# Kernel optimization log

Hardware: AMD Instinct MI355X
Metric: run time of the kernel (lower is better)

## Reference

```python
import jax, jax.numpy as jnp
import numpy as np

N = 50000
D = 128
E = 625000
EPS = 1e-15
BALL_EPS = 1e-5


def _logmap0(x, c):
    # Poincare ball log map at origin: artanh(sqrt(c)||x||) * x / (sqrt(c)||x||)
    sqrt_c = jnp.sqrt(c)
    xn = jnp.clip(jnp.linalg.norm(x, axis=-1, keepdims=True), EPS)
    arg = jnp.clip(sqrt_c * xn, -1.0 + BALL_EPS, 1.0 - BALL_EPS)
    return jnp.arctanh(arg) * x / (sqrt_c * xn)


def _expmap0(u, c):
    # Poincare ball exp map at origin: tanh(sqrt(c)||u||) * u / (sqrt(c)||u||)
    sqrt_c = jnp.sqrt(c)
    un = jnp.clip(jnp.linalg.norm(u, axis=-1, keepdims=True), EPS)
    return jnp.tanh(sqrt_c * un) * u / (sqrt_c * un)


def setup_inputs() -> dict:
    key = jax.random.key(0)
    ks = jax.random.split(key, 10)
    scale = 0.01  # keep points well inside the Poincare ball
    node_embeddings = jax.random.normal(ks[0], (N, D), jnp.float32) * scale
    hist1 = jax.random.normal(ks[1], (N, D), jnp.float32) * scale
    hist2 = jax.random.normal(ks[2], (N, D), jnp.float32) * scale
    hist3 = jax.random.normal(ks[3], (N, D), jnp.float32) * scale
    lin_w = jax.random.normal(ks[4], (D, D), jnp.float32) * (1.0 / np.sqrt(D))
    lin_b = jnp.zeros((D,), jnp.float32)
    conv_w = jax.random.normal(ks[5], (D, D, 3), jnp.float32) * (1.0 / np.sqrt(3 * D))
    conv_b = jnp.zeros((D,), jnp.float32)
    curvature = jnp.array([-1.0], jnp.float32)
    edge_src = jax.random.randint(ks[6], (E,), 0, N, jnp.int32)
    edge_dst = jax.random.randint(ks[7], (E,), 0, N, jnp.int32)
    return {
        'node_embeddings': node_embeddings,
        'hist1': hist1, 'hist2': hist2, 'hist3': hist3,
        'lin_w': lin_w, 'lin_b': lin_b,
        'conv_w': conv_w, 'conv_b': conv_b,
        'curvature': curvature,
        'edge_src': edge_src, 'edge_dst': edge_dst,
    }


def reference(node_embeddings, hist1, hist2, hist3, lin_w, lin_b,
              conv_w, conv_b, curvature, edge_src, edge_dst):
    c = jnp.abs(curvature[0])

    # --- HyperbolicDiffusionGraphConv ---
    tangent = _logmap0(node_embeddings, c)                       # [N, D]
    transformed = tangent @ lin_w.T + lin_b                      # [N, D]
    msgs = transformed[edge_src]                                 # [E, D] gather
    summed = jax.ops.segment_sum(msgs, edge_dst, num_segments=N)  # [N, D] scatter
    deg = jax.ops.segment_sum(jnp.ones((E,), jnp.float32), edge_dst, num_segments=N)
    neigh = jnp.where(deg[:, None] > 0, summed / jnp.clip(deg[:, None], 1.0), 0.0)
    current_emb = _expmap0(neigh, c)                             # [N, D]

    # --- HyperbolicDilatedCausalConv (3-step history, kernel_size=3 -> length 1) ---
    tangent_cur = _logmap0(current_emb, c)
    th = jnp.stack([_logmap0(hist1, c), _logmap0(hist2, c), _logmap0(hist3, c)], axis=2)  # [N, D, 3]
    # Conv1d(D -> D, k=3) on length-3 input reduces to a single contraction.
    conv_out = jnp.einsum('nik,oik->no', th, conv_w) + conv_b    # [N, D]
    return _expmap0(conv_out + tangent_cur, c)
```

## Files before the change

### kernel.cpp

```cpp
#include <hip/hip_runtime.h>

#define N_NODES 50000
#define DIM 128
#define N_EDGES 625000
#define EBLK2 1221
#define SLOTS 96

#define SC_BLOCKS 12500
#define PK_BLOCKS 256
#define ZR_BLOCKS 196
#define SETUP_BLOCKS (SC_BLOCKS + PK_BLOCKS + ZR_BLOCKS)

typedef float f32x4 __attribute__((ext_vector_type(4)));
typedef short s16x8 __attribute__((ext_vector_type(8)));

union U8 { unsigned short us[8]; uint4 v; };

__device__ __forceinline__ unsigned short f2bf(float f) {
    unsigned u = __builtin_bit_cast(unsigned, f);
    unsigned r = (u + 0x7fffu + ((u >> 16) & 1u)) >> 16;
    return (unsigned short)r;
}
__device__ __forceinline__ float lo_bf(unsigned u) {
    return __builtin_bit_cast(float, u << 16);
}
__device__ __forceinline__ float hi_bf(unsigned u) {
    return __builtin_bit_cast(float, u & 0xffff0000u);
}

__device__ __forceinline__ void gload_lds16(const unsigned short* g, unsigned short* l) {
    __builtin_amdgcn_global_load_lds(
        (const __attribute__((address_space(1))) void*)g,
        (__attribute__((address_space(3))) void*)l, 16, 0, 0);
}

__device__ __forceinline__ float logmap_scale(float ss, float sc) {
    float xn = fmaxf(sqrtf(ss), 1e-15f);
    float arg = fminf(sc * xn, 1.0f - 1e-5f);
    if (arg < 0.25f) {
        float z2 = arg * arg;
        return 1.0f + z2 * (0.33333333f + z2 * (0.2f + z2 * 0.14285715f));
    }
    float at = 0.5f * log1pf(2.0f * arg / (1.0f - arg));
    return at / (sc * xn);
}

__global__ __launch_bounds__(256) void k_setup(
    const float* __restrict__ node, const float* __restrict__ h1,
    const float* __restrict__ h2, const float* __restrict__ h3,
    const float* __restrict__ lin_w, const float* __restrict__ conv_w,
    const float* __restrict__ curv,
    unsigned short* __restrict__ node_t, unsigned short* __restrict__ A,
    unsigned short* __restrict__ Wt, int* __restrict__ cnt) {
    int b = blockIdx.x;
    int tid = threadIdx.x;
    if (b < SC_BLOCKS) {
        int row = b * 16 + (tid >> 4);
        int g = tid & 15;
        int a = row / N_NODES;
        int n = row - a * N_NODES;
        const float* src = (a == 0) ? node : (a == 1) ? h1 : (a == 2) ? h2 : h3;
        const float4* p = (const float4*)&src[n * DIM + g * 8];
        float4 x0 = p[0], x1 = p[1];
        float ss = x0.x * x0.x + x0.y * x0.y + x0.z * x0.z + x0.w * x0.w
                 + x1.x * x1.x + x1.y * x1.y + x1.z * x1.z + x1.w * x1.w;
        ss += __shfl_xor(ss, 1, 64);
        ss += __shfl_xor(ss, 2, 64);
        ss += __shfl_xor(ss, 4, 64);
        ss += __shfl_xor(ss, 8, 64);
        float c = fabsf(curv[0]);
        float s = logmap_scale(ss, sqrtf(c));
        U8 u;
        u.us[0] = f2bf(x0.x * s); u.us[1] = f2bf(x0.y * s);
        u.us[2] = f2bf(x0.z * s); u.us[3] = f2bf(x0.w * s);
        u.us[4] = f2bf(x1.x * s); u.us[5] = f2bf(x1.y * s);
        u.us[6] = f2bf(x1.z * s); u.us[7] = f2bf(x1.w * s);
        if (a == 0) {
            *(uint4*)&node_t[n * DIM + g * 8] = u.v;
        } else {
            *(uint4*)&A[n * 512 + a * 128 + g * 8] = u.v;
        }
    } else if (b < SC_BLOCKS + PK_BLOCKS) {
        int idx = (b - SC_BLOCKS) * 256 + tid;
        int o = idx >> 9;
        int k = idx & 511;
        float v;
        if (k < 128) {
            v = lin_w[o * 128 + k];
        } else {
            int kk = (k - 128) >> 7;
            int i = (k - 128) & 127;
            v = conv_w[o * 384 + i * 3 + kk];
        }
        Wt[idx] = f2bf(v);
    } else {
        int i = (b - SC_BLOCKS - PK_BLOCKS) * 256 + tid;
        if (i < N_NODES) cnt[i] = 0;
    }
}

__global__ void k_bucket(const int* __restrict__ esrc, const int* __restrict__ edst,
                         int* __restrict__ cnt, unsigned short* __restrict__ slots) {
    int e0 = blockIdx.x * 512 + threadIdx.x;
    int e1 = e0 + 256;
    int d0 = -1, d1 = -1, v0 = 0, v1 = 0;
    if (e0 < N_EDGES) { d0 = edst[e0]; v0 = esrc[e0]; }
    if (e1 < N_EDGES) { d1 = edst[e1]; v1 = esrc[e1]; }
    if (d0 >= 0) {
        int pos = __hip_atomic_fetch_add(&cnt[d0], 1, __ATOMIC_RELAXED,
                                         __HIP_MEMORY_SCOPE_AGENT);
        if (pos < SLOTS) slots[d0 * SLOTS + pos] = (unsigned short)v0;
    }
    if (d1 >= 0) {
        int pos = __hip_atomic_fetch_add(&cnt[d1], 1, __ATOMIC_RELAXED,
                                         __HIP_MEMORY_SCOPE_AGENT);
        if (pos < SLOTS) slots[d1 * SLOTS + pos] = (unsigned short)v1;
    }
}

__global__ __launch_bounds__(256) void k_gather(
    const unsigned short* __restrict__ slots, const int* __restrict__ cnt,
    const unsigned short* __restrict__ node_t, unsigned short* __restrict__ A) {
    int n = blockIdx.x * 8 + (threadIdx.x >> 5);
    int lane = threadIdx.x & 31;
    int ctrue = cnt[n];
    int c = ctrue < SLOTS ? ctrue : SLOTS;
    const unsigned short* row = &slots[n * SLOTS];
    float p0 = 0.f, p1 = 0.f, p2 = 0.f, p3 = 0.f;
    float q0 = 0.f, q1 = 0.f, q2 = 0.f, q3 = 0.f;
    for (int base = 0; base < c; base += 32) {
        int rem = c - base;
        int m = rem < 32 ? rem : 32;
        int my = (int)row[base + (lane < m ? lane : m - 1)];
        for (int i = 0; i < m; i += 8) {
            int i1 = i + 1 < m ? i + 1 : m - 1;
            int i2 = i + 2 < m ? i + 2 : m - 1;
            int i3 = i + 3 < m ? i + 3 : m - 1;
            int i4 = i + 4 < m ? i + 4 : m - 1;
            int i5 = i + 5 < m ? i + 5 : m - 1;
            int i6 = i + 6 < m ? i + 6 : m - 1;
            int i7 = i + 7 < m ? i + 7 : m - 1;
            int s0 = __shfl(my, i, 32),  s1 = __shfl(my, i1, 32);
            int s2 = __shfl(my, i2, 32), s3 = __shfl(my, i3, 32);
            int s4 = __shfl(my, i4, 32), s5 = __shfl(my, i5, 32);
            int s6 = __shfl(my, i6, 32), s7 = __shfl(my, i7, 32);
            uint2 u0 = *(const uint2*)&node_t[s0 * DIM + lane * 4];
            uint2 u1 = *(const uint2*)&node_t[s1 * DIM + lane * 4];
            uint2 u2 = *(const uint2*)&node_t[s2 * DIM + lane * 4];
            uint2 u3 = *(const uint2*)&node_t[s3 * DIM + lane * 4];
            uint2 u4 = *(const uint2*)&node_t[s4 * DIM + lane * 4];
            uint2 u5 = *(const uint2*)&node_t[s5 * DIM + lane * 4];
            uint2 u6 = *(const uint2*)&node_t[s6 * DIM + lane * 4];
            uint2 u7 = *(const uint2*)&node_t[s7 * DIM + lane * 4];
            p0 += lo_bf(u0.x); p1 += hi_bf(u0.x); p2 += lo_bf(u0.y); p3 += hi_bf(u0.y);
            if (i + 1 < m) { q0 += lo_bf(u1.x); q1 += hi_bf(u1.x); q2 += lo_bf(u1.y); q3 += hi_bf(u1.y); }
            if (i + 2 < m) { p0 += lo_bf(u2.x); p1 += hi_bf(u2.x); p2 += lo_bf(u2.y); p3 += hi_bf(u2.y); }
            if (i + 3 < m) { q0 += lo_bf(u3.x); q1 += hi_bf(u3.x); q2 += lo_bf(u3.y); q3 += hi_bf(u3.y); }
            if (i + 4 < m) { p0 += lo_bf(u4.x); p1 += hi_bf(u4.x); p2 += lo_bf(u4.y); p3 += hi_bf(u4.y); }
            if (i + 5 < m) { q0 += lo_bf(u5.x); q1 += hi_bf(u5.x); q2 += lo_bf(u5.y); q3 += hi_bf(u5.y); }
            if (i + 6 < m) { p0 += lo_bf(u6.x); p1 += hi_bf(u6.x); p2 += lo_bf(u6.y); p3 += hi_bf(u6.y); }
            if (i + 7 < m) { q0 += lo_bf(u7.x); q1 += hi_bf(u7.x); q2 += lo_bf(u7.y); q3 += hi_bf(u7.y); }
        }
    }
    float t0 = p0 + q0, t1 = p1 + q1, t2 = p2 + q2, t3 = p3 + q3;
    float inv = (ctrue > 0) ? 1.0f / (float)ctrue : 0.0f;
    unsigned short o0 = f2bf(t0 * inv), o1 = f2bf(t1 * inv);
    unsigned short o2 = f2bf(t2 * inv), o3 = f2bf(t3 * inv);
    uint2 ov;
    ov.x = (unsigned)o0 | ((unsigned)o1 << 16);
    ov.y = (unsigned)o2 | ((unsigned)o3 << 16);
    *(uint2*)&A[n * 512 + lane * 4] = ov;
}

#define RB 64
#define BK 64
__global__ __launch_bounds__(256) void k_gemm(
    const unsigned short* __restrict__ A, const int* __restrict__ deg,
    const unsigned short* __restrict__ Wt,
    const float* __restrict__ lin_b, const float* __restrict__ conv_b,
    const float* __restrict__ curv, float* __restrict__ out) {
    __shared__ __align__(16) unsigned short As[2][RB * BK];
    __shared__ __align__(16) unsigned short Bs[2][128 * BK];
    int tid = threadIdx.x;
    int n0 = blockIdx.x * RB;
    int w = tid >> 6;
    int lane = tid & 63;
    int ml = lane & 15;
    int q = lane >> 4;
    int lr = lane >> 3;
    int lj = lane & 7;

    f32x4 acc[8];
    #pragma unroll
    for (int i = 0; i < 8; ++i) acc[i] = (f32x4){0.f, 0.f, 0.f, 0.f};

    #pragma unroll
    for (int t = 0; t < 2; ++t) {
        int m = t * 4 + w;
        int r = m * 8 + lr;
        int jg = lj ^ (r & 7);
        gload_lds16(A + (n0 + r) * 512 + jg * 8, &As[0][m * 512]);
    }
    #pragma unroll
    for (int t = 0; t < 4; ++t) {
        int m = t * 4 + w;
        int r = m * 8 + lr;
        int jg = lj ^ (r & 7);
        gload_lds16(Wt + r * 512 + jg * 8, &Bs[0][m * 512]);
    }

    #pragma unroll
    for (int kk = 0; kk < 8; ++kk) {
        int cur = kk & 1;
        __syncthreads();
        if (kk < 7) {
            int nb = cur ^ 1;
            #pragma unroll
            for (int t = 0; t < 2; ++t) {
                int m = t * 4 + w;
                int r = m * 8 + lr;
                int jg = lj ^ (r & 7);
                gload_lds16(A + (n0 + r) * 512 + (kk + 1) * 64 + jg * 8, &As[nb][m * 512]);
            }
            #pragma unroll
            for (int t = 0; t < 4; ++t) {
                int m = t * 4 + w;
                int r = m * 8 + lr;
                int jg = lj ^ (r & 7);
                gload_lds16(Wt + r * 512 + (kk + 1) * 64 + jg * 8, &Bs[nb][m * 512]);
            }
        }
        __builtin_amdgcn_s_setprio(1);
        #pragma unroll
        for (int ks = 0; ks < 2; ++ks) {
            int ca = ((ks * 4 + q) ^ (ml & 7)) * 8;
            s16x8 a = *(const s16x8*)&As[cur][(w * 16 + ml) * BK + ca];
            #pragma unroll
            for (int ct = 0; ct < 8; ++ct) {
                s16x8 bb = *(const s16x8*)&Bs[cur][(ct * 16 + ml) * BK + ca];
                acc[ct] = __builtin_amdgcn_mfma_f32_16x16x32_bf16(a, bb, acc[ct], 0, 0, 0);
            }
        }
        __builtin_amdgcn_s_setprio(0);
    }

    float c = fabsf(curv[0]);
    float sc = sqrtf(c);
    float cb[8], lb[8];
    #pragma unroll
    for (int ct = 0; ct < 8; ++ct) {
        cb[ct] = conv_b[ct * 16 + ml];
        lb[ct] = lin_b[ct * 16 + ml];
    }
    #pragma unroll
    for (int r = 0; r < 4; ++r) {
        int n = n0 + w * 16 + q * 4 + r;
        bool valid = (n < N_NODES);
        float dgf = 0.f;
        if (valid) dgf = (deg[n] > 0) ? 1.0f : 0.0f;
        float y[8];
        float ssq = 0.f;
        #pragma unroll
        for (int ct = 0; ct < 8; ++ct) {
            float v = acc[ct][r] + cb[ct] + dgf * lb[ct];
            y[ct] = v;
            ssq += v * v;
        }
        ssq += __shfl_xor(ssq, 1, 64);
        ssq += __shfl_xor(ssq, 2, 64);
        ssq += __shfl_xor(ssq, 4, 64);
        ssq += __shfl_xor(ssq, 8, 64);
        float un = fmaxf(sqrtf(ssq), 1e-15f);
        float z = sc * un;
        float os;
        if (z < 0.25f) {
            float z2 = z * z;
            os = 1.0f + z2 * (-0.33333333f + z2 * (0.13333333f - z2 * 0.053968254f));
        } else {
            os = tanhf(z) / z;
        }
        if (valid) {
            #pragma unroll
            for (int ct = 0; ct < 8; ++ct)
                out[n * DIM + ct * 16 + ml] = y[ct] * os;
        }
    }
}

extern "C" void kernel_launch(void* const* d_in, const int* in_sizes, int n_in,
                              void* d_out, int out_size, void* d_ws, size_t ws_size,
                              hipStream_t stream) {
    (void)in_sizes; (void)n_in; (void)out_size; (void)ws_size;
    const float* node   = (const float*)d_in[0];
    const float* h1     = (const float*)d_in[1];
    const float* h2     = (const float*)d_in[2];
    const float* h3     = (const float*)d_in[3];
    const float* lin_w  = (const float*)d_in[4];
    const float* lin_b  = (const float*)d_in[5];
    const float* conv_w = (const float*)d_in[6];
    const float* conv_b = (const float*)d_in[7];
    const float* curv   = (const float*)d_in[8];
    const int* esrc = (const int*)d_in[9];
    const int* edst = (const int*)d_in[10];
    float* out = (float*)d_out;

    char* ws = (char*)d_ws;
    unsigned short* A = (unsigned short*)ws;
    unsigned short* node_t = (unsigned short*)(ws + 51200000);
    unsigned short* Wt = (unsigned short*)(ws + 64000000);
    int* cnt = (int*)(ws + 64131072);
    unsigned short* slots = (unsigned short*)(ws + 64331072);

    hipLaunchKernelGGL(k_setup, dim3(SETUP_BLOCKS), dim3(256), 0, stream,
                       node, h1, h2, h3, lin_w, conv_w, curv,
                       node_t, A, Wt, cnt);
    hipLaunchKernelGGL(k_bucket, dim3(EBLK2), dim3(256), 0, stream,
                       esrc, edst, cnt, slots);
    hipLaunchKernelGGL(k_gather, dim3(6250), dim3(256), 0, stream,
                       slots, cnt, node_t, A);
    hipLaunchKernelGGL(k_gemm, dim3((N_NODES + RB - 1) / RB), dim3(256), 0, stream,
                       A, cnt, Wt, lin_b, conv_b, curv, out);
}
```

Before: 238.8 us.

## Pad atomic counters, widen setup rows, one edge per thread, double GEMM row tile

Per-node edge counters are padded to a 16-int stride so atomics on different nodes fall on separate cache lines. The bucket kernel now handles one edge per thread. The setup kernel processes 16 floats per thread with 8 threads per row. The GEMM row tile grows from 64 to 128, with each wave computing two 16-row MFMA tiles so every loaded B fragment is reused twice. The trade-offs are more accumulator registers, fewer GEMM blocks, and a larger counter array that must be zeroed.

```diff
diff --git a/kernel.cpp b/kernel.cpp
--- a/kernel.cpp
+++ b/kernel.cpp
@@ -3,12 +3,13 @@
 #define N_NODES 50000
 #define DIM 128
 #define N_EDGES 625000
-#define EBLK2 1221
+#define EBLK 2442
 #define SLOTS 96
-
-#define SC_BLOCKS 12500
+#define CSTRIDE 16
+
+#define SC_BLOCKS 6250
 #define PK_BLOCKS 256
-#define ZR_BLOCKS 196
+#define ZR_BLOCKS 3125
 #define SETUP_BLOCKS (SC_BLOCKS + PK_BLOCKS + ZR_BLOCKS)
 
 typedef float f32x4 __attribute__((ext_vector_type(4)));
@@ -55,30 +56,37 @@
     int b = blockIdx.x;
     int tid = threadIdx.x;
     if (b < SC_BLOCKS) {
-        int row = b * 16 + (tid >> 4);
-        int g = tid & 15;
+        int row = b * 32 + (tid >> 3);
+        int g = tid & 7;
         int a = row / N_NODES;
         int n = row - a * N_NODES;
         const float* src = (a == 0) ? node : (a == 1) ? h1 : (a == 2) ? h2 : h3;
-        const float4* p = (const float4*)&src[n * DIM + g * 8];
-        float4 x0 = p[0], x1 = p[1];
+        const float4* p = (const float4*)&src[n * DIM + g * 16];
+        float4 x0 = p[0], x1 = p[1], x2 = p[2], x3 = p[3];
         float ss = x0.x * x0.x + x0.y * x0.y + x0.z * x0.z + x0.w * x0.w
-                 + x1.x * x1.x + x1.y * x1.y + x1.z * x1.z + x1.w * x1.w;
+                 + x1.x * x1.x + x1.y * x1.y + x1.z * x1.z + x1.w * x1.w
+                 + x2.x * x2.x + x2.y * x2.y + x2.z * x2.z + x2.w * x2.w
+                 + x3.x * x3.x + x3.y * x3.y + x3.z * x3.z + x3.w * x3.w;
         ss += __shfl_xor(ss, 1, 64);
         ss += __shfl_xor(ss, 2, 64);
         ss += __shfl_xor(ss, 4, 64);
-        ss += __shfl_xor(ss, 8, 64);
         float c = fabsf(curv[0]);
         float s = logmap_scale(ss, sqrtf(c));
-        U8 u;
+        U8 u, v;
         u.us[0] = f2bf(x0.x * s); u.us[1] = f2bf(x0.y * s);
         u.us[2] = f2bf(x0.z * s); u.us[3] = f2bf(x0.w * s);
         u.us[4] = f2bf(x1.x * s); u.us[5] = f2bf(x1.y * s);
         u.us[6] = f2bf(x1.z * s); u.us[7] = f2bf(x1.w * s);
+        v.us[0] = f2bf(x2.x * s); v.us[1] = f2bf(x2.y * s);
+        v.us[2] = f2bf(x2.z * s); v.us[3] = f2bf(x2.w * s);
+        v.us[4] = f2bf(x3.x * s); v.us[5] = f2bf(x3.y * s);
+        v.us[6] = f2bf(x3.z * s); v.us[7] = f2bf(x3.w * s);
         if (a == 0) {
-            *(uint4*)&node_t[n * DIM + g * 8] = u.v;
+            *(uint4*)&node_t[n * DIM + g * 16] = u.v;
+            *(uint4*)&node_t[n * DIM + g * 16 + 8] = v.v;
         } else {
-            *(uint4*)&A[n * 512 + a * 128 + g * 8] = u.v;
+            *(uint4*)&A[n * 512 + a * 128 + g * 16] = u.v;
+            *(uint4*)&A[n * 512 + a * 128 + g * 16 + 8] = v.v;
         }
     } else if (b < SC_BLOCKS + PK_BLOCKS) {
         int idx = (b - SC_BLOCKS) * 256 + tid;
@@ -95,27 +103,18 @@
         Wt[idx] = f2bf(v);
     } else {
         int i = (b - SC_BLOCKS - PK_BLOCKS) * 256 + tid;
-        if (i < N_NODES) cnt[i] = 0;
+        if (i < N_NODES * CSTRIDE) cnt[i] = 0;
     }
 }
 
 __global__ void k_bucket(const int* __restrict__ esrc, const int* __restrict__ edst,
                          int* __restrict__ cnt, unsigned short* __restrict__ slots) {
-    int e0 = blockIdx.x * 512 + threadIdx.x;
-    int e1 = e0 + 256;
-    int d0 = -1, d1 = -1, v0 = 0, v1 = 0;
-    if (e0 < N_EDGES) { d0 = edst[e0]; v0 = esrc[e0]; }
-    if (e1 < N_EDGES) { d1 = edst[e1]; v1 = esrc[e1]; }
-    if (d0 >= 0) {
-        int pos = __hip_atomic_fetch_add(&cnt[d0], 1, __ATOMIC_RELAXED,
-                                         __HIP_MEMORY_SCOPE_AGENT);
-        if (pos < SLOTS) slots[d0 * SLOTS + pos] = (unsigned short)v0;
-    }
-    if (d1 >= 0) {
-        int pos = __hip_atomic_fetch_add(&cnt[d1], 1, __ATOMIC_RELAXED,
-                                         __HIP_MEMORY_SCOPE_AGENT);
-        if (pos < SLOTS) slots[d1 * SLOTS + pos] = (unsigned short)v1;
-    }
+    int e = blockIdx.x * 256 + threadIdx.x;
+    if (e >= N_EDGES) return;
+    int d = edst[e];
+    int pos = __hip_atomic_fetch_add(&cnt[d * CSTRIDE], 1, __ATOMIC_RELAXED,
+                                     __HIP_MEMORY_SCOPE_AGENT);
+    if (pos < SLOTS) slots[d * SLOTS + pos] = (unsigned short)esrc[e];
 }
 
 __global__ __launch_bounds__(256) void k_gather(
@@ -123,7 +122,7 @@
     const unsigned short* __restrict__ node_t, unsigned short* __restrict__ A) {
     int n = blockIdx.x * 8 + (threadIdx.x >> 5);
     int lane = threadIdx.x & 31;
-    int ctrue = cnt[n];
+    int ctrue = cnt[n * CSTRIDE];
     int c = ctrue < SLOTS ? ctrue : SLOTS;
     const unsigned short* row = &slots[n * SLOTS];
     float p0 = 0.f, p1 = 0.f, p2 = 0.f, p3 = 0.f;
@@ -172,7 +171,7 @@
     *(uint2*)&A[n * 512 + lane * 4] = ov;
 }
 
-#define RB 64
+#define RB 128
 #define BK 64
 __global__ __launch_bounds__(256) void k_gemm(
     const unsigned short* __restrict__ A, const int* __restrict__ deg,
@@ -190,12 +189,14 @@
     int lr = lane >> 3;
     int lj = lane & 7;
 
-    f32x4 acc[8];
-    #pragma unroll
-    for (int i = 0; i < 8; ++i) acc[i] = (f32x4){0.f, 0.f, 0.f, 0.f};
-
-    #pragma unroll
-    for (int t = 0; t < 2; ++t) {
+    f32x4 acc[2][8];
+    #pragma unroll
+    for (int rt = 0; rt < 2; ++rt)
+        #pragma unroll
+        for (int i = 0; i < 8; ++i) acc[rt][i] = (f32x4){0.f, 0.f, 0.f, 0.f};
+
+    #pragma unroll
+    for (int t = 0; t < 4; ++t) {
         int m = t * 4 + w;
         int r = m * 8 + lr;
         int jg = lj ^ (r & 7);
@@ -216,7 +217,7 @@
         if (kk < 7) {
             int nb = cur ^ 1;
             #pragma unroll
-            for (int t = 0; t < 2; ++t) {
+            for (int t = 0; t < 4; ++t) {
                 int m = t * 4 + w;
                 int r = m * 8 + lr;
                 int jg = lj ^ (r & 7);
@@ -234,11 +235,13 @@
         #pragma unroll
         for (int ks = 0; ks < 2; ++ks) {
             int ca = ((ks * 4 + q) ^ (ml & 7)) * 8;
-            s16x8 a = *(const s16x8*)&As[cur][(w * 16 + ml) * BK + ca];
+            s16x8 a0 = *(const s16x8*)&As[cur][(w * 32 + ml) * BK + ca];
+            s16x8 a1 = *(const s16x8*)&As[cur][(w * 32 + 16 + ml) * BK + ca];
             #pragma unroll
             for (int ct = 0; ct < 8; ++ct) {
                 s16x8 bb = *(const s16x8*)&Bs[cur][(ct * 16 + ml) * BK + ca];
-                acc[ct] = __builtin_amdgcn_mfma_f32_16x16x32_bf16(a, bb, acc[ct], 0, 0, 0);
+                acc[0][ct] = __builtin_amdgcn_mfma_f32_16x16x32_bf16(a0, bb, acc[0][ct], 0, 0, 0);
+                acc[1][ct] = __builtin_amdgcn_mfma_f32_16x16x32_bf16(a1, bb, acc[1][ct], 0, 0, 0);
             }
         }
         __builtin_amdgcn_s_setprio(0);
@@ -253,36 +256,39 @@
         lb[ct] = lin_b[ct * 16 + ml];
     }
     #pragma unroll
-    for (int r = 0; r < 4; ++r) {
-        int n = n0 + w * 16 + q * 4 + r;
-        bool valid = (n < N_NODES);
-        float dgf = 0.f;
-        if (valid) dgf = (deg[n] > 0) ? 1.0f : 0.0f;
-        float y[8];
-        float ssq = 0.f;
+    for (int rt = 0; rt < 2; ++rt) {
         #pragma unroll
-        for (int ct = 0; ct < 8; ++ct) {
-            float v = acc[ct][r] + cb[ct] + dgf * lb[ct];
-            y[ct] = v;
-            ssq += v * v;
-        }
-        ssq += __shfl_xor(ssq, 1, 64);
-        ssq += __shfl_xor(ssq, 2, 64);
-        ssq += __shfl_xor(ssq, 4, 64);
-        ssq += __shfl_xor(ssq, 8, 64);
-        float un = fmaxf(sqrtf(ssq), 1e-15f);
-        float z = sc * un;
-        float os;
-        if (z < 0.25f) {
-            float z2 = z * z;
-            os = 1.0f + z2 * (-0.33333333f + z2 * (0.13333333f - z2 * 0.053968254f));
-        } else {
-            os = tanhf(z) / z;
-        }
-        if (valid) {
+        for (int r = 0; r < 4; ++r) {
+            int n = n0 + w * 32 + rt * 16 + q * 4 + r;
+            bool valid = (n < N_NODES);
+            float dgf = 0.f;
+            if (valid) dgf = (deg[n * CSTRIDE] > 0) ? 1.0f : 0.0f;
+            float y[8];
+            float ssq = 0.f;
             #pragma unroll
-            for (int ct = 0; ct < 8; ++ct)
-                out[n * DIM + ct * 16 + ml] = y[ct] * os;
+            for (int ct = 0; ct < 8; ++ct) {
+                float v = acc[rt][ct][r] + cb[ct] + dgf * lb[ct];
+                y[ct] = v;
+                ssq += v * v;
+            }
+            ssq += __shfl_xor(ssq, 1, 64);
+            ssq += __shfl_xor(ssq, 2, 64);
+            ssq += __shfl_xor(ssq, 4, 64);
+            ssq += __shfl_xor(ssq, 8, 64);
+            float un = fmaxf(sqrtf(ssq), 1e-15f);
+            float z = sc * un;
+            float os;
+            if (z < 0.25f) {
+                float z2 = z * z;
+                os = 1.0f + z2 * (-0.33333333f + z2 * (0.13333333f - z2 * 0.053968254f));
+            } else {
+                os = tanhf(z) / z;
+            }
+            if (valid) {
+                #pragma unroll
+                for (int ct = 0; ct < 8; ++ct)
+                    out[n * DIM + ct * 16 + ml] = y[ct] * os;
+            }
         }
     }
 }
@@ -309,12 +315,12 @@
     unsigned short* node_t = (unsigned short*)(ws + 51200000);
     unsigned short* Wt = (unsigned short*)(ws + 64000000);
     int* cnt = (int*)(ws + 64131072);
-    unsigned short* slots = (unsigned short*)(ws + 64331072);
+    unsigned short* slots = (unsigned short*)(ws + 67331072);
 
     hipLaunchKernelGGL(k_setup, dim3(SETUP_BLOCKS), dim3(256), 0, stream,
                        node, h1, h2, h3, lin_w, conv_w, curv,
                        node_t, A, Wt, cnt);
-    hipLaunchKernelGGL(k_bucket, dim3(EBLK2), dim3(256), 0, stream,
+    hipLaunchKernelGGL(k_bucket, dim3(EBLK), dim3(256), 0, stream,
                        esrc, edst, cnt, slots);
     hipLaunchKernelGGL(k_gather, dim3(6250), dim3(256), 0, stream,
                        slots, cnt, node_t, A);
```

After: 232.7 us. 1.03x faster.
